# Optimization experiments

Hardware: AMD Instinct MI355X
Metric: run time of the kernel (lower is better)

The kernel has to match this reference:

```python
import jax, jax.numpy as jnp
import numpy as np

BSZ, KW, D_MODEL, TEXT_DIM, VOCAB = 128, 8, 768, 512, 49408
EPS = 1e-8  # matches torch F.cosine_similarity eps


def setup_inputs() -> dict:
    key = jax.random.key(0)
    k1, k2, k3, k4 = jax.random.split(key, 4)
    return {
        "keywords": jax.random.normal(k1, (BSZ, KW, D_MODEL), dtype=jnp.float32),
        "W_proj": jax.random.normal(k2, (D_MODEL, TEXT_DIM), dtype=jnp.float32) * (1.0 / np.sqrt(D_MODEL)),
        "b_proj": jax.random.normal(k3, (TEXT_DIM,), dtype=jnp.float32) * 0.02,
        "W_emb": jax.random.normal(k4, (VOCAB, TEXT_DIM), dtype=jnp.float32) * 0.02,
    }


def reference(keywords, W_proj, b_proj, W_emb):
    # linear_proj: [B, K, d_model] -> [B, K, text_dim]
    kw = jnp.einsum("bkm,md->bkd", keywords, W_proj) + b_proj
    # cosine similarity of each keyword against the full token-embedding table
    kw_n = kw / jnp.maximum(jnp.linalg.norm(kw, axis=-1, keepdims=True), EPS)
    emb_n = W_emb / jnp.maximum(jnp.linalg.norm(W_emb, axis=-1, keepdims=True), EPS)
    cos_score = jnp.einsum("bkd,vd->bkv", kw_n, emb_n)  # [B, K, V]
    # soft VQ: subword probability over vocab
    subword_prob = jax.nn.softmax(cos_score, axis=-1)
    # soft assignment against the (frozen) embedding table
    kw_out = jnp.einsum("bkv,vd->bkd", subword_prob, W_emb)  # [B, K, text_dim]
    return kw_out, subword_prob, cos_score
```

## Files before the change

kernel.cpp:

```cpp
#include <hip/hip_runtime.h>

#define VOC 49408
#define TD 512
#define DM 768
#define NCOLG2 193
#define PV_S 32

typedef __attribute__((ext_vector_type(8))) short bf16x8;
typedef __attribute__((ext_vector_type(4))) short bf16x4;
typedef __attribute__((ext_vector_type(4))) float f32x4;

__device__ __forceinline__ unsigned short f2bf(float f) {
  unsigned int u = __float_as_uint(f);
  u += 0x7fffu + ((u >> 16) & 1u);
  return (unsigned short)(u >> 16);
}

__device__ __forceinline__ void gload16(const void* g, const void* l) {
  __builtin_amdgcn_global_load_lds(
      (const __attribute__((address_space(1))) void*)g,
      (__attribute__((address_space(3))) void*)l, 16, 0, 0);
}

__global__ __launch_bounds__(256) void k_proj(const float* __restrict__ kw,
                                              const float* __restrict__ Wp,
                                              const float* __restrict__ bp,
                                              unsigned short* __restrict__ kwn) {
  __shared__ float row_lds[4 * DM];
  __shared__ float rsum[4][4];
  __shared__ float rinv_s[4];
  const int t = threadIdx.x;
  const int rb = blockIdx.x * 4;
  for (int i = 0; i < 12; ++i) {
    int idx = i * 256 + t;
    row_lds[idx] = kw[(size_t)rb * DM + idx];
  }
  __syncthreads();
  float acc[4][2] = {};
  for (int m = 0; m < DM; ++m) {
    float w0 = Wp[m * TD + t];
    float w1 = Wp[m * TD + t + 256];
#pragma unroll
    for (int r = 0; r < 4; ++r) {
      float kv = row_lds[r * DM + m];
      acc[r][0] = fmaf(kv, w0, acc[r][0]);
      acc[r][1] = fmaf(kv, w1, acc[r][1]);
    }
  }
  const float b0 = bp[t], b1 = bp[t + 256];
  float p[4];
#pragma unroll
  for (int r = 0; r < 4; ++r) {
    acc[r][0] += b0;
    acc[r][1] += b1;
    p[r] = acc[r][0] * acc[r][0] + acc[r][1] * acc[r][1];
  }
#pragma unroll
  for (int off = 32; off; off >>= 1) {
#pragma unroll
    for (int r = 0; r < 4; ++r) p[r] += __shfl_down(p[r], off);
  }
  const int lane = t & 63, wv = t >> 6;
  if (lane == 0) {
#pragma unroll
    for (int r = 0; r < 4; ++r) rsum[r][wv] = p[r];
  }
  __syncthreads();
  if (t < 4) {
    float s = rsum[t][0] + rsum[t][1] + rsum[t][2] + rsum[t][3];
    rinv_s[t] = 1.0f / fmaxf(sqrtf(s), 1e-8f);
  }
  __syncthreads();
#pragma unroll
  for (int r = 0; r < 4; ++r) {
    float ri = rinv_s[r];
    kwn[(size_t)(rb + r) * TD + t] = f2bf(acc[r][0] * ri);
    kwn[(size_t)(rb + r) * TD + t + 256] = f2bf(acc[r][1] * ri);
  }
}

__global__ __launch_bounds__(256) void k_norms(const float* __restrict__ We,
                                               unsigned short* __restrict__ embB,
                                               float* __restrict__ rnormv) {
  const int t = threadIdx.x;
  const int lane = t & 63, w = t >> 6;
  const int v = blockIdx.x * 4 + w;
  const float* rowp = We + (size_t)v * TD;
  float4 a = *(const float4*)(rowp + lane * 8);
  float4 b = *(const float4*)(rowp + lane * 8 + 4);
  bf16x8 o;
  o[0] = (short)f2bf(a.x); o[1] = (short)f2bf(a.y);
  o[2] = (short)f2bf(a.z); o[3] = (short)f2bf(a.w);
  o[4] = (short)f2bf(b.x); o[5] = (short)f2bf(b.y);
  o[6] = (short)f2bf(b.z); o[7] = (short)f2bf(b.w);
  *(bf16x8*)(embB + (size_t)v * TD + lane * 8) = o;
  float ss = a.x * a.x + a.y * a.y + a.z * a.z + a.w * a.w +
             b.x * b.x + b.y * b.y + b.z * b.z + b.w * b.w;
#pragma unroll
  for (int off = 1; off < 64; off <<= 1) ss += __shfl_xor(ss, off);
  if (lane == 0) rnormv[v] = 1.0f / fmaxf(sqrtf(ss), 1e-8f);
}

__global__ __launch_bounds__(256) void k_transpose(const unsigned short* __restrict__ embB,
                                                   unsigned short* __restrict__ embT) {
  __shared__ unsigned short tile[64 * 72];
  const int t = threadIdx.x;
  const int d0 = blockIdx.x * 64, v0 = blockIdx.y * 64;
#pragma unroll
  for (int p = 0; p < 2; ++p) {
    int vl = p * 32 + (t >> 3), ch = t & 7;
    *(bf16x8*)&tile[vl * 72 + ch * 8] =
        *(const bf16x8*)(embB + (size_t)(v0 + vl) * TD + d0 + ch * 8);
  }
  __syncthreads();
#pragma unroll
  for (int p = 0; p < 2; ++p) {
    int dl = p * 32 + (t >> 3), vch = t & 7;
    bf16x8 o;
#pragma unroll
    for (int i = 0; i < 8; ++i) o[i] = (short)tile[(vch * 8 + i) * 72 + dl];
    *(bf16x8*)(embT + (size_t)(d0 + dl) * VOC + v0 + vch * 8) = o;
  }
}

__global__ __launch_bounds__(512, 2) void k_cos(const unsigned short* __restrict__ kwn,
                                                const unsigned short* __restrict__ embB,
                                                const float* __restrict__ rnormv,
                                                float* __restrict__ cosd,
                                                float* __restrict__ partial) {
  __shared__ unsigned short As[256 * 64];
  __shared__ unsigned short Bs[256 * 64];
  __shared__ float rs[2][256];
  const int t = threadIdx.x;
  const int lane = t & 63, w = t >> 6;
  const int wr = w & 3, wc = w >> 2;
  const int g = lane >> 4, l15 = lane & 15;
  const int rowg = blockIdx.x;
  const int colg = blockIdx.y;

  const int rl = lane >> 3;
  const int bsl = (lane & 7) ^ rl;

  f32x4 acc[4][8];
#pragma unroll
  for (int mi = 0; mi < 4; ++mi)
#pragma unroll
    for (int ni = 0; ni < 8; ++ni)
#pragma unroll
      for (int j = 0; j < 4; ++j) acc[mi][ni][j] = 0.0f;

  for (int kt = 0; kt < 8; ++kt) {
#pragma unroll
    for (int i = 0; i < 4; ++i) {
      gload16(kwn + (size_t)(rowg * 256 + i * 64 + w * 8 + rl) * TD + kt * 64 + bsl * 8,
              (const void*)(As + (i * 64 + w * 8) * 64));
      gload16(embB + (size_t)(colg * 256 + i * 64 + w * 8 + rl) * TD + kt * 64 + bsl * 8,
              (const void*)(Bs + (i * 64 + w * 8) * 64));
    }
    __syncthreads();
#pragma unroll
    for (int ks = 0; ks < 2; ++ks) {
      const int ch = (((ks * 4 + g) ^ (l15 & 7)) << 3);
      bf16x8 a[4];
#pragma unroll
      for (int mi = 0; mi < 4; ++mi)
        a[mi] = *(const bf16x8*)&As[(wr * 64 + mi * 16 + l15) * 64 + ch];
#pragma unroll
      for (int ni = 0; ni < 8; ++ni) {
        bf16x8 b = *(const bf16x8*)&Bs[(wc * 128 + ni * 16 + l15) * 64 + ch];
#pragma unroll
        for (int mi = 0; mi < 4; ++mi)
          acc[mi][ni] = __builtin_amdgcn_mfma_f32_16x16x32_bf16(a[mi], b, acc[mi][ni], 0, 0, 0);
      }
    }
    __syncthreads();
  }

  const size_t rowbase = (size_t)rowg * 256 + wr * 64;
  const int colbase = colg * 256 + wc * 128;
  float rnv[8];
#pragma unroll
  for (int ni = 0; ni < 8; ++ni) rnv[ni] = rnormv[colbase + ni * 16 + l15];
#pragma unroll
  for (int mi = 0; mi < 4; ++mi) {
    float es[4] = {0.f, 0.f, 0.f, 0.f};
#pragma unroll
    for (int ni = 0; ni < 8; ++ni) {
#pragma unroll
      for (int j = 0; j < 4; ++j) {
        float c = acc[mi][ni][j] * rnv[ni];
        cosd[(rowbase + mi * 16 + g * 4 + j) * VOC + colbase + ni * 16 + l15] = c;
        es[j] += __expf(c);
      }
    }
#pragma unroll
    for (int j = 0; j < 4; ++j) {
      float e = es[j];
      e += __shfl_xor(e, 1);
      e += __shfl_xor(e, 2);
      e += __shfl_xor(e, 4);
      e += __shfl_xor(e, 8);
      if (l15 == 0) rs[wc][wr * 64 + mi * 16 + g * 4 + j] = e;
    }
  }
  __syncthreads();
  if (t < 256) {
    float srow = rs[0][t] + rs[1][t];
    partial[(size_t)colg * 1024 + rowg * 256 + t] = srow;
  }
}

__global__ __launch_bounds__(256) void k_denom(const float* __restrict__ partial,
                                               float* __restrict__ rdenom) {
  const int t = threadIdx.x;
  const int lane = t & 63, w = t >> 6;
  const int row = blockIdx.x * 4 + w;
  float s = 0.f;
  for (int c = lane; c < NCOLG2; c += 64) s += partial[(size_t)c * 1024 + row];
#pragma unroll
  for (int off = 1; off < 64; off <<= 1) s += __shfl_xor(s, off);
  if (lane == 0) rdenom[row] = 1.0f / s;
}

__global__ __launch_bounds__(256, 2) void k_pv(const float* __restrict__ cosd,
                                               const unsigned short* __restrict__ embT,
                                               const float* __restrict__ rdenom,
                                               float* __restrict__ prob,
                                               float* __restrict__ kpart) {
  __shared__ unsigned short As[128 * 64];
  __shared__ unsigned short Bs[256 * 64];
  const int t = threadIdx.x;
  const int lane = t & 63, w = t >> 6;
  const int wr = w >> 1, wc = w & 1;
  const int g = lane >> 4, l15 = lane & 15;
  const int rowg = blockIdx.x;
  const int colg = blockIdx.y;
  const int s = blockIdx.z;
  const int t0 = s * 24 + (s < 4 ? s : 4);
  const int t1 = t0 + 24 + (s < 4 ? 1 : 0);

  const int ar = t >> 1, ah = t & 1;
  const int grow = rowg * 128 + ar;
  const float rdv = rdenom[grow];
  const float* cbase = cosd + (size_t)grow * VOC + ah * 4;
  float* pbase = prob + (size_t)grow * VOC + ah * 4;

  const int brow_l = lane >> 3;
  const int bsl = (lane & 7) ^ brow_l;

  f32x4 acc[4][8];
#pragma unroll
  for (int mi = 0; mi < 4; ++mi)
#pragma unroll
    for (int ni = 0; ni < 8; ++ni)
#pragma unroll
      for (int j = 0; j < 4; ++j) acc[mi][ni][j] = 0.0f;

  float4 cc[8];
  {
    const float* cp = cbase + (size_t)t0 * 64;
#pragma unroll
    for (int i = 0; i < 8; ++i) cc[i] = *(const float4*)(cp + i * 8);
  }

  for (int kt = t0; kt < t1; ++kt) {
    const int v0 = kt * 64;
    __syncthreads();

#pragma unroll
    for (int i = 0; i < 8; ++i) {
      gload16(embT + (size_t)(colg * 256 + i * 32 + w * 8 + brow_l) * VOC + v0 + bsl * 8,
              (const void*)(Bs + (i * 32 + w * 8) * 64));
    }

    float4 px[8];
#pragma unroll
    for (int i = 0; i < 8; ++i) {
      px[i].x = __expf(cc[i].x) * rdv;
      px[i].y = __expf(cc[i].y) * rdv;
      px[i].z = __expf(cc[i].z) * rdv;
      px[i].w = __expf(cc[i].w) * rdv;
    }
    if (colg == 0) {
#pragma unroll
      for (int i = 0; i < 8; ++i) *(float4*)(pbase + v0 + i * 8) = px[i];
    }
#pragma unroll
    for (int i = 0; i < 8; ++i) {
      bf16x4 b4;
      b4[0] = (short)f2bf(px[i].x);
      b4[1] = (short)f2bf(px[i].y);
      b4[2] = (short)f2bf(px[i].z);
      b4[3] = (short)f2bf(px[i].w);
      *(bf16x4*)&As[ar * 64 + ((i ^ (ar & 7)) << 3) + ah * 4] = b4;
    }

    if (kt + 1 < t1) {
      const float* cp = cbase + (size_t)(kt + 1) * 64;
#pragma unroll
      for (int i = 0; i < 8; ++i) cc[i] = *(const float4*)(cp + i * 8);
    }

    __syncthreads();

#pragma unroll
    for (int ks = 0; ks < 2; ++ks) {
      const int ch = (((ks * 4 + g) ^ (l15 & 7)) << 3);
      bf16x8 a[4];
#pragma unroll
      for (int mi = 0; mi < 4; ++mi)
        a[mi] = *(const bf16x8*)&As[(wr * 64 + mi * 16 + l15) * 64 + ch];
#pragma unroll
      for (int ni = 0; ni < 8; ++ni) {
        bf16x8 b = *(const bf16x8*)&Bs[(wc * 128 + ni * 16 + l15) * 64 + ch];
#pragma unroll
        for (int mi = 0; mi < 4; ++mi)
          acc[mi][ni] = __builtin_amdgcn_mfma_f32_16x16x32_bf16(a[mi], b, acc[mi][ni], 0, 0, 0);
      }
    }
  }

#pragma unroll
  for (int mi = 0; mi < 4; ++mi)
#pragma unroll
    for (int ni = 0; ni < 8; ++ni)
#pragma unroll
      for (int j = 0; j < 4; ++j)
        kpart[((size_t)s * 1024 + rowg * 128 + wr * 64 + mi * 16 + g * 4 + j) * TD +
              colg * 256 + wc * 128 + ni * 16 + l15] = acc[mi][ni][j];
}

__global__ __launch_bounds__(256) void k_kwout(const float* __restrict__ kpart,
                                               float* __restrict__ outp) {
  const int gid = blockIdx.x * 256 + threadIdx.x;
  float4 s = {0.f, 0.f, 0.f, 0.f};
#pragma unroll
  for (int sp = 0; sp < PV_S; ++sp) {
    float4 v = *(const float4*)(kpart + (size_t)sp * 524288 + gid * 4);
    s.x += v.x; s.y += v.y; s.z += v.z; s.w += v.w;
  }
  *(float4*)(outp + gid * 4) = s;
}

extern "C" void kernel_launch(void* const* d_in, const int* in_sizes, int n_in,
                              void* d_out, int out_size, void* d_ws, size_t ws_size,
                              hipStream_t stream) {
  const float* kw = (const float*)d_in[0];
  const float* Wp = (const float*)d_in[1];
  const float* bp = (const float*)d_in[2];
  const float* We = (const float*)d_in[3];
  float* out = (float*)d_out;
  char* ws = (char*)d_ws;

  unsigned short* embT = (unsigned short*)ws;
  unsigned short* embB = (unsigned short*)(ws + 50593792);
  unsigned short* kwn = (unsigned short*)(ws + 101187584);
  float* rnormv = (float*)(ws + 102236160);
  float* partial = (float*)(ws + 102433792);
  float* rdenom = (float*)(ws + 103224320);
  float* kpart = (float*)(ws + 103228416);

  float* kwout = out;
  float* prob = out + 524288;
  float* cosd = out + 51118080;

  hipLaunchKernelGGL(k_proj, dim3(256), dim3(256), 0, stream, kw, Wp, bp, kwn);
  hipLaunchKernelGGL(k_norms, dim3(12352), dim3(256), 0, stream, We, embB, rnormv);
  hipLaunchKernelGGL(k_transpose, dim3(8, 772), dim3(256), 0, stream, embB, embT);
  hipLaunchKernelGGL(k_cos, dim3(4, NCOLG2), dim3(512), 0, stream, kwn, embB, rnormv,
                     cosd, partial);
  hipLaunchKernelGGL(k_denom, dim3(256), dim3(256), 0, stream, partial, rdenom);
  hipLaunchKernelGGL(k_pv, dim3(8, 2, PV_S), dim3(256), 0, stream, cosd, embT, rdenom,
                     prob, kpart);
  hipLaunchKernelGGL(k_kwout, dim3(512), dim3(256), 0, stream, kpart, kwout);
}
```

Before: 397.2 us.

## Double-buffer LDS in cos and PV GEMMs and enlarge PV row tile

Adds LDS double buffering to k_cos and k_pv, so the global-to-LDS loads for the next K tile are issued before the MFMA work on the current tile and one barrier per iteration is removed. k_pv moves to 512-thread blocks covering 256 rows, which halves how often each embT tile is re-read from memory. The prob writes are now split between the two column groups by tile parity instead of always falling to colg 0. The cost is 128KB of LDS per block, which may limit occupancy to one block per CU despite the launch bounds.

```diff
diff --git a/kernel.cpp b/kernel.cpp
--- a/kernel.cpp
+++ b/kernel.cpp
@@ -128,9 +128,7 @@
                                                 const float* __restrict__ rnormv,
                                                 float* __restrict__ cosd,
                                                 float* __restrict__ partial) {
-  __shared__ unsigned short As[256 * 64];
-  __shared__ unsigned short Bs[256 * 64];
-  __shared__ float rs[2][256];
+  __shared__ unsigned short smem[2][2][256 * 64];
   const int t = threadIdx.x;
   const int lane = t & 63, w = t >> 6;
   const int wr = w & 3, wc = w >> 2;
@@ -149,25 +147,37 @@
 #pragma unroll
       for (int j = 0; j < 4; ++j) acc[mi][ni][j] = 0.0f;
 
+  const unsigned short* Ag = kwn + (size_t)(rowg * 256 + w * 8 + rl) * TD + bsl * 8;
+  const unsigned short* Bg = embB + (size_t)(colg * 256 + w * 8 + rl) * TD + bsl * 8;
+
+#pragma unroll
+  for (int i = 0; i < 4; ++i) {
+    gload16(Ag + (size_t)(i * 64) * TD, (const void*)(&smem[0][0][(i * 64 + w * 8) * 64]));
+    gload16(Bg + (size_t)(i * 64) * TD, (const void*)(&smem[0][1][(i * 64 + w * 8) * 64]));
+  }
+  __syncthreads();
+
   for (int kt = 0; kt < 8; ++kt) {
-#pragma unroll
-    for (int i = 0; i < 4; ++i) {
-      gload16(kwn + (size_t)(rowg * 256 + i * 64 + w * 8 + rl) * TD + kt * 64 + bsl * 8,
-              (const void*)(As + (i * 64 + w * 8) * 64));
-      gload16(embB + (size_t)(colg * 256 + i * 64 + w * 8 + rl) * TD + kt * 64 + bsl * 8,
-              (const void*)(Bs + (i * 64 + w * 8) * 64));
-    }
-    __syncthreads();
+    const int buf = kt & 1;
+    if (kt < 7) {
+#pragma unroll
+      for (int i = 0; i < 4; ++i) {
+        gload16(Ag + (size_t)(i * 64) * TD + (kt + 1) * 64,
+                (const void*)(&smem[buf ^ 1][0][(i * 64 + w * 8) * 64]));
+        gload16(Bg + (size_t)(i * 64) * TD + (kt + 1) * 64,
+                (const void*)(&smem[buf ^ 1][1][(i * 64 + w * 8) * 64]));
+      }
+    }
 #pragma unroll
     for (int ks = 0; ks < 2; ++ks) {
       const int ch = (((ks * 4 + g) ^ (l15 & 7)) << 3);
       bf16x8 a[4];
 #pragma unroll
       for (int mi = 0; mi < 4; ++mi)
-        a[mi] = *(const bf16x8*)&As[(wr * 64 + mi * 16 + l15) * 64 + ch];
+        a[mi] = *(const bf16x8*)&smem[buf][0][(wr * 64 + mi * 16 + l15) * 64 + ch];
 #pragma unroll
       for (int ni = 0; ni < 8; ++ni) {
-        bf16x8 b = *(const bf16x8*)&Bs[(wc * 128 + ni * 16 + l15) * 64 + ch];
+        bf16x8 b = *(const bf16x8*)&smem[buf][1][(wc * 128 + ni * 16 + l15) * 64 + ch];
 #pragma unroll
         for (int mi = 0; mi < 4; ++mi)
           acc[mi][ni] = __builtin_amdgcn_mfma_f32_16x16x32_bf16(a[mi], b, acc[mi][ni], 0, 0, 0);
@@ -176,6 +186,7 @@
     __syncthreads();
   }
 
+  float (*rs)[256] = (float(*)[256]) & smem[0][0][0];
   const size_t rowbase = (size_t)rowg * 256 + wr * 64;
   const int colbase = colg * 256 + wc * 128;
   float rnv[8];
@@ -222,16 +233,15 @@
   if (lane == 0) rdenom[row] = 1.0f / s;
 }
 
-__global__ __launch_bounds__(256, 2) void k_pv(const float* __restrict__ cosd,
+__global__ __launch_bounds__(512, 2) void k_pv(const float* __restrict__ cosd,
                                                const unsigned short* __restrict__ embT,
                                                const float* __restrict__ rdenom,
                                                float* __restrict__ prob,
                                                float* __restrict__ kpart) {
-  __shared__ unsigned short As[128 * 64];
-  __shared__ unsigned short Bs[256 * 64];
+  __shared__ unsigned short smem[2][2][256 * 64];
   const int t = threadIdx.x;
   const int lane = t & 63, w = t >> 6;
-  const int wr = w >> 1, wc = w & 1;
+  const int wr = w & 3, wc = w >> 2;
   const int g = lane >> 4, l15 = lane & 15;
   const int rowg = blockIdx.x;
   const int colg = blockIdx.y;
@@ -240,13 +250,13 @@
   const int t1 = t0 + 24 + (s < 4 ? 1 : 0);
 
   const int ar = t >> 1, ah = t & 1;
-  const int grow = rowg * 128 + ar;
+  const int grow = rowg * 256 + ar;
   const float rdv = rdenom[grow];
   const float* cbase = cosd + (size_t)grow * VOC + ah * 4;
   float* pbase = prob + (size_t)grow * VOC + ah * 4;
 
-  const int brow_l = lane >> 3;
-  const int bsl = (lane & 7) ^ brow_l;
+  const int rl = lane >> 3;
+  const int bsl = (lane & 7) ^ rl;
 
   f32x4 acc[4][8];
 #pragma unroll
@@ -263,61 +273,82 @@
     for (int i = 0; i < 8; ++i) cc[i] = *(const float4*)(cp + i * 8);
   }
 
+#pragma unroll
+  for (int i = 0; i < 4; ++i) {
+    gload16(embT + (size_t)(colg * 256 + i * 64 + w * 8 + rl) * VOC + t0 * 64 + bsl * 8,
+            (const void*)(&smem[0][1][(i * 64 + w * 8) * 64]));
+  }
+  {
+    const bool wp = (colg == (t0 & 1));
+#pragma unroll
+    for (int i = 0; i < 8; ++i) {
+      float4 px;
+      px.x = __expf(cc[i].x) * rdv;
+      px.y = __expf(cc[i].y) * rdv;
+      px.z = __expf(cc[i].z) * rdv;
+      px.w = __expf(cc[i].w) * rdv;
+      if (wp) *(float4*)(pbase + (size_t)t0 * 64 + i * 8) = px;
+      bf16x4 b4;
+      b4[0] = (short)f2bf(px.x);
+      b4[1] = (short)f2bf(px.y);
+      b4[2] = (short)f2bf(px.z);
+      b4[3] = (short)f2bf(px.w);
+      *(bf16x4*)&smem[0][0][ar * 64 + ((i ^ (ar & 7)) << 3) + ah * 4] = b4;
+    }
+  }
+  if (t0 + 1 < t1) {
+    const float* cp = cbase + (size_t)(t0 + 1) * 64;
+#pragma unroll
+    for (int i = 0; i < 8; ++i) cc[i] = *(const float4*)(cp + i * 8);
+  }
+  __syncthreads();
+
   for (int kt = t0; kt < t1; ++kt) {
-    const int v0 = kt * 64;
-    __syncthreads();
-
-#pragma unroll
-    for (int i = 0; i < 8; ++i) {
-      gload16(embT + (size_t)(colg * 256 + i * 32 + w * 8 + brow_l) * VOC + v0 + bsl * 8,
-              (const void*)(Bs + (i * 32 + w * 8) * 64));
-    }
-
-    float4 px[8];
-#pragma unroll
-    for (int i = 0; i < 8; ++i) {
-      px[i].x = __expf(cc[i].x) * rdv;
-      px[i].y = __expf(cc[i].y) * rdv;
-      px[i].z = __expf(cc[i].z) * rdv;
-      px[i].w = __expf(cc[i].w) * rdv;
-    }
-    if (colg == 0) {
-#pragma unroll
-      for (int i = 0; i < 8; ++i) *(float4*)(pbase + v0 + i * 8) = px[i];
-    }
-#pragma unroll
-    for (int i = 0; i < 8; ++i) {
-      bf16x4 b4;
-      b4[0] = (short)f2bf(px[i].x);
-      b4[1] = (short)f2bf(px[i].y);
-      b4[2] = (short)f2bf(px[i].z);
-      b4[3] = (short)f2bf(px[i].w);
-      *(bf16x4*)&As[ar * 64 + ((i ^ (ar & 7)) << 3) + ah * 4] = b4;
-    }
-
+    const int buf = (kt - t0) & 1;
     if (kt + 1 < t1) {
-      const float* cp = cbase + (size_t)(kt + 1) * 64;
-#pragma unroll
-      for (int i = 0; i < 8; ++i) cc[i] = *(const float4*)(cp + i * 8);
-    }
-
-    __syncthreads();
-
+#pragma unroll
+      for (int i = 0; i < 4; ++i) {
+        gload16(embT + (size_t)(colg * 256 + i * 64 + w * 8 + rl) * VOC + (kt + 1) * 64 + bsl * 8,
+                (const void*)(&smem[buf ^ 1][1][(i * 64 + w * 8) * 64]));
+      }
+      const bool wp = (colg == ((kt + 1) & 1));
+#pragma unroll
+      for (int i = 0; i < 8; ++i) {
+        float4 px;
+        px.x = __expf(cc[i].x) * rdv;
+        px.y = __expf(cc[i].y) * rdv;
+        px.z = __expf(cc[i].z) * rdv;
+        px.w = __expf(cc[i].w) * rdv;
+        if (wp) *(float4*)(pbase + (size_t)(kt + 1) * 64 + i * 8) = px;
+        bf16x4 b4;
+        b4[0] = (short)f2bf(px.x);
+        b4[1] = (short)f2bf(px.y);
+        b4[2] = (short)f2bf(px.z);
+        b4[3] = (short)f2bf(px.w);
+        *(bf16x4*)&smem[buf ^ 1][0][ar * 64 + ((i ^ (ar & 7)) << 3) + ah * 4] = b4;
+      }
+      if (kt + 2 < t1) {
+        const float* cp = cbase + (size_t)(kt + 2) * 64;
+#pragma unroll
+        for (int i = 0; i < 8; ++i) cc[i] = *(const float4*)(cp + i * 8);
+      }
+    }
 #pragma unroll
     for (int ks = 0; ks < 2; ++ks) {
       const int ch = (((ks * 4 + g) ^ (l15 & 7)) << 3);
       bf16x8 a[4];
 #pragma unroll
       for (int mi = 0; mi < 4; ++mi)
-        a[mi] = *(const bf16x8*)&As[(wr * 64 + mi * 16 + l15) * 64 + ch];
+        a[mi] = *(const bf16x8*)&smem[buf][0][(wr * 64 + mi * 16 + l15) * 64 + ch];
 #pragma unroll
       for (int ni = 0; ni < 8; ++ni) {
-        bf16x8 b = *(const bf16x8*)&Bs[(wc * 128 + ni * 16 + l15) * 64 + ch];
+        bf16x8 b = *(const bf16x8*)&smem[buf][1][(wc * 128 + ni * 16 + l15) * 64 + ch];
 #pragma unroll
         for (int mi = 0; mi < 4; ++mi)
           acc[mi][ni] = __builtin_amdgcn_mfma_f32_16x16x32_bf16(a[mi], b, acc[mi][ni], 0, 0, 0);
       }
     }
+    __syncthreads();
   }
 
 #pragma unroll
@@ -326,7 +357,7 @@
     for (int ni = 0; ni < 8; ++ni)
 #pragma unroll
       for (int j = 0; j < 4; ++j)
-        kpart[((size_t)s * 1024 + rowg * 128 + wr * 64 + mi * 16 + g * 4 + j) * TD +
+        kpart[((size_t)s * 1024 + rowg * 256 + wr * 64 + mi * 16 + g * 4 + j) * TD +
               colg * 256 + wc * 128 + ni * 16 + l15] = acc[mi][ni][j];
 }
 
@@ -370,7 +401,7 @@
   hipLaunchKernelGGL(k_cos, dim3(4, NCOLG2), dim3(512), 0, stream, kwn, embB, rnormv,
                      cosd, partial);
   hipLaunchKernelGGL(k_denom, dim3(256), dim3(256), 0, stream, partial, rdenom);
-  hipLaunchKernelGGL(k_pv, dim3(8, 2, PV_S), dim3(256), 0, stream, cosd, embT, rdenom,
+  hipLaunchKernelGGL(k_pv, dim3(4, 2, PV_S), dim3(512), 0, stream, cosd, embT, rdenom,
                      prob, kpart);
   hipLaunchKernelGGL(k_kwout, dim3(512), dim3(256), 0, stream, kpart, kwout);
 }
```

After: 377.7 us. 1.05x faster.
